# Kernel tuning notes

Hardware: AMD Instinct MI355X
Metric: run time of the kernel (lower is better)

The kernel has to match this reference:

```python
import jax, jax.numpy as jnp
import numpy as np

B_SZ, NX, IN_DIM = 32, 16384, 3
DIM, J, MODE, RANK, FC_DIM, OUT_DIM, N_LAYERS = 64, 16, 128, 4, 128, 1, 3


def setup_inputs() -> dict:
    key = jax.random.key(0)
    ks = jax.random.split(key, 20)
    scale = 1.0 / (MODE * MODE)
    s_out = 1.0 / MODE
    x = jax.random.normal(ks[0], (B_SZ, NX, IN_DIM), jnp.float32)
    bases = jax.random.normal(ks[1], (NX, MODE), jnp.float32) / np.sqrt(NX)
    wbases = jax.random.normal(ks[2], (NX, MODE), jnp.float32) / np.sqrt(NX)
    product = bases.T @ wbases  # (MODE_out, MODE_in)
    D_out = np.sqrt(s_out) * jax.random.uniform(ks[3], (J, MODE), jnp.float32)
    D_in = np.sqrt(s_out) * jax.random.uniform(ks[4], (J, MODE), jnp.float32)
    A = s_out * jax.random.uniform(ks[5], (J, RANK, MODE), jnp.float32)
    Bm = s_out * jax.random.uniform(ks[6], (J, RANK, MODE), jnp.float32)
    W_sp = scale * jax.random.normal(ks[7], (N_LAYERS, DIM, DIM, J), jnp.float32)
    W_conv = jax.random.normal(ks[8], (N_LAYERS, DIM, DIM), jnp.float32) / np.sqrt(DIM)
    b_conv = jnp.zeros((N_LAYERS, DIM), jnp.float32)
    W0 = jax.random.normal(ks[9], (IN_DIM, DIM), jnp.float32) / np.sqrt(IN_DIM)
    b0 = jnp.zeros((DIM,), jnp.float32)
    W1 = jax.random.normal(ks[10], (DIM, FC_DIM), jnp.float32) / np.sqrt(DIM)
    b1 = jnp.zeros((FC_DIM,), jnp.float32)
    W2 = jax.random.normal(ks[11], (FC_DIM, OUT_DIM), jnp.float32) / np.sqrt(FC_DIM)
    b2 = jnp.zeros((OUT_DIM,), jnp.float32)
    return {"x": x, "bases": bases, "wbases": wbases, "product": product,
            "D_out": D_out, "D_in": D_in, "A": A, "Bm": Bm,
            "W_sp": W_sp, "W_conv": W_conv, "b_conv": b_conv,
            "W0": W0, "b0": b0, "W1": W1, "b1": b1, "W2": W2, "b2": b2}


def reference(x, bases, wbases, product, D_out, D_in, A, Bm, W_sp, W_conv, b_conv,
              W0, b0, W1, b1, W2, b2):
    # fc0: (b, nx, in_dim) -> (b, nx, dim), then channel-first (b, dim, nx)
    h = jnp.swapaxes(x @ W0 + b0, 1, 2)
    # H construction: diag outer-products + low-rank A^T B update (mask_mode=0 so full add)
    H = D_out[:, :, None] * D_in[:, None, :] * product[None] \
        + jnp.einsum('jrk,jrl->jkl', A, Bm)  # (J, MODE, MODE)
    for i in range(N_LAYERS):
        xh = jnp.einsum('bcx,xk->bck', h, wbases)          # spectral transform
        xh1 = jnp.einsum('jkl,bil->bijk', H, xh)           # H mixing
        y = jnp.einsum('ioj,bijk->bok', W_sp[i], xh1)      # channel/kernel contraction
        x1 = jnp.einsum('bck,xk->bcx', y, bases)           # inverse transform
        x2 = jnp.einsum('oc,bcx->box', W_conv[i], h) + b_conv[i][None, :, None]
        h = x1 + x2
        if i != N_LAYERS - 1:
            h = jax.nn.gelu(h, approximate=False)
    h = jnp.swapaxes(h, 1, 2)  # (b, nx, dim)
    h = jax.nn.gelu(h @ W1 + b1, approximate=False)
    return h @ W2 + b2
```

## Files before the change

### kernel.cpp

```cpp
#include <hip/hip_runtime.h>
#include <hip/hip_bf16.h>
#include <math.h>

#define B_SZ   32
#define NXX    16384
#define IN_DIM 3
#define DIM    64
#define JM     16
#define MODE   128
#define RANKK  4
#define FC_DIM 128
#define N_LAY  3

typedef __attribute__((ext_vector_type(8))) short bf16x8;
typedef __attribute__((ext_vector_type(4))) float f32x4;
typedef unsigned short u16;

__device__ __forceinline__ float gelu_fast(float v) {
    float p = v * (0.7978845608f + 0.0356774081f * v * v);
    float e = __expf(-2.f * p);
    return v * __builtin_amdgcn_rcpf(1.f + e);
}
__device__ __forceinline__ u16 to_bf16(float v) {
    __hip_bfloat16 b = __float2bfloat16(v);
    return *(u16*)&b;
}

__global__ __launch_bounds__(256) void k_zero(float* __restrict__ p, int n) {
    int i = blockIdx.x * 256 + threadIdx.x;
    if (i < n) p[i] = 0.f;
}

__global__ __launch_bounds__(256) void k_build_H(
        const float* __restrict__ Dout, const float* __restrict__ Din,
        const float* __restrict__ product, const float* __restrict__ A,
        const float* __restrict__ Bm, u16* __restrict__ Hbf) {
    int idx = blockIdx.x * 256 + threadIdx.x;
    int j = idx >> 14;
    int k = (idx >> 7) & 127;
    int l = idx & 127;
    float v = Dout[j * MODE + k] * Din[j * MODE + l] * product[k * MODE + l];
#pragma unroll
    for (int r = 0; r < RANKK; ++r)
        v += A[(j * RANKK + r) * MODE + k] * Bm[(j * RANKK + r) * MODE + l];
    Hbf[idx] = to_bf16(v);
}

__global__ __launch_bounds__(256) void k_setup_wst(
        const float* __restrict__ Wsp, u16* __restrict__ WsT) {
    int idx = blockIdx.x * 256 + threadIdx.x;
    int i = idx & 63, o = (idx >> 6) & 63, j = (idx >> 12) & 15, lay = idx >> 16;
    WsT[idx] = to_bf16(Wsp[(((size_t)lay * 64 + i) * 64 + o) * 16 + j]);
}

__global__ __launch_bounds__(256) void k_setup_bases(
        const float* __restrict__ bases, u16* __restrict__ bh) {
    int idx = blockIdx.x * 256 + threadIdx.x;
    int x = idx >> 7, k = idx & 127;
    size_t off = (size_t)(k >> 3) * 131072 + (size_t)x * 8 + (k & 7);
    bh[off] = to_bf16(bases[idx]);
}

__global__ __launch_bounds__(256) void k_setup_wbT(
        const float* __restrict__ wb, u16* __restrict__ Th) {
    __shared__ float tile[32][33];
    int bx = blockIdx.x, bl = blockIdx.y;
    int t = threadIdx.x;
    int i = t >> 5, jj = t & 31;
#pragma unroll
    for (int r = 0; r < 4; ++r)
        tile[i + r * 8][jj] = wb[(size_t)(bx * 32 + i + r * 8) * MODE + bl * 32 + jj];
    __syncthreads();
#pragma unroll
    for (int r = 0; r < 4; ++r) {
        int l = bl * 32 + i + r * 8;
        int x = bx * 32 + jj;
        Th[(size_t)l * NXX + x] = to_bf16(tile[jj][i + r * 8]);
    }
}

__global__ __launch_bounds__(256) void k_setup_w1t(
        const float* __restrict__ W1, u16* __restrict__ wh) {
    int i = blockIdx.x * 256 + threadIdx.x;
    int f = i >> 6, c = i & 63;
    wh[i] = to_bf16(W1[c * FC_DIM + f]);
}

__global__ __launch_bounds__(256) void k_fc0(
        const float* __restrict__ x, const float* __restrict__ W0,
        const float* __restrict__ b0, u16* __restrict__ hh) {
    __shared__ float w0s[IN_DIM * DIM + DIM];
    int t = threadIdx.x;
    if (t < IN_DIM * DIM) w0s[t] = W0[t];
    if (t < DIM) w0s[IN_DIM * DIM + t] = b0[t];
    __syncthreads();
    int b = blockIdx.y;
    int xi = blockIdx.x * 32 + (t >> 3);
    int c8 = (t & 7) * 8;
    const float* xp = x + ((size_t)b * NXX + xi) * IN_DIM;
    float x0 = xp[0], x1 = xp[1], x2 = xp[2];
    u16 rh[8];
#pragma unroll
    for (int i = 0; i < 8; ++i) {
        int c = c8 + i;
        float v = x0 * w0s[c] + x1 * w0s[DIM + c] + x2 * w0s[2 * DIM + c]
                + w0s[3 * DIM + c];
        rh[i] = to_bf16(v);
    }
    size_t o = ((size_t)(b << 14) + xi) * 64 + c8;
    *(ushort4*)(hh + o)     = make_ushort4(rh[0], rh[1], rh[2], rh[3]);
    *(ushort4*)(hh + o + 4) = make_ushort4(rh[4], rh[5], rh[6], rh[7]);
}

#define SPAD 72
__global__ __launch_bounds__(256) void k_spectral_mfma(
        const u16* __restrict__ Hh,
        const u16* __restrict__ Wh,
        float* __restrict__ xh) {
    __shared__ u16 Ash[64 * SPAD];
    int t = threadIdx.x;
    int wave = t >> 6, lane = t & 63, quad = lane >> 4, l16 = lane & 15;
    int b = blockIdx.x;
    int x0 = blockIdx.y * 512;
    int cq = (t & 15) * 4;
    int xq = (t >> 4) * 4;
    int colw = (xq + ((t & 7) << 3)) & 63;
    const u16* srch = Hh + ((size_t)(b << 14) + x0 + xq) * 64 + cq;
    int l0 = wave * 32;
    const u16* w0h = Wh + (size_t)(l0 + l16) * NXX + x0;
    const u16* w1h = Wh + (size_t)(l0 + 16 + l16) * NXX + x0;
    f32x4 acc[4][2] = {};
    for (int kt = 0; kt < 512; kt += 64) {
        __syncthreads();
        {
            const u16* s = srch + (size_t)kt * 64;
            ushort4 r0 = *(const ushort4*)(s);
            ushort4 r1 = *(const ushort4*)(s + 64);
            ushort4 r2 = *(const ushort4*)(s + 128);
            ushort4 r3 = *(const ushort4*)(s + 192);
            *(ushort4*)&Ash[(cq + 0) * SPAD + colw] = make_ushort4(r0.x, r1.x, r2.x, r3.x);
            *(ushort4*)&Ash[(cq + 1) * SPAD + colw] = make_ushort4(r0.y, r1.y, r2.y, r3.y);
            *(ushort4*)&Ash[(cq + 2) * SPAD + colw] = make_ushort4(r0.z, r1.z, r2.z, r3.z);
            *(ushort4*)&Ash[(cq + 3) * SPAD + colw] = make_ushort4(r0.w, r1.w, r2.w, r3.w);
        }
        __syncthreads();
#pragma unroll
        for (int k0 = 0; k0 < 64; k0 += 32) {
            bf16x8 afh[4];
#pragma unroll
            for (int ct = 0; ct < 4; ++ct) {
                int rr = ct * 16 + l16;
                int ro = rr * SPAD + (((k0 + quad * 8) + (((rr >> 2) & 7) << 3)) & 63);
                afh[ct] = *(const bf16x8*)&Ash[ro];
            }
            int go = kt + k0 + quad * 8;
            bf16x8 b0h = *(const bf16x8*)(w0h + go);
            bf16x8 b1h = *(const bf16x8*)(w1h + go);
#pragma unroll
            for (int ct = 0; ct < 4; ++ct) {
                acc[ct][0] = __builtin_amdgcn_mfma_f32_16x16x32_bf16(afh[ct], b0h, acc[ct][0], 0, 0, 0);
                acc[ct][1] = __builtin_amdgcn_mfma_f32_16x16x32_bf16(afh[ct], b1h, acc[ct][1], 0, 0, 0);
            }
        }
    }
    float* xb = xh + (size_t)(b << 6) * 128;
#pragma unroll
    for (int ct = 0; ct < 4; ++ct)
#pragma unroll
        for (int lt = 0; lt < 2; ++lt)
#pragma unroll
            for (int r = 0; r < 4; ++r)
                atomicAdd(xb + (size_t)(ct * 16 + quad * 4 + r) * 128 + l0 + lt * 16 + l16,
                          acc[ct][lt][r]);
}

#define XPAD 136
#define TPAD 72
__global__ __launch_bounds__(256) void k_hmix_mfma(
        const float* __restrict__ xh, const u16* __restrict__ Hbf,
        const u16* __restrict__ WsT, float* __restrict__ y, int lay) {
    __shared__ u16 xsb[64 * XPAD];
    __shared__ u16 Ts[128 * TPAD];
    int t = threadIdx.x;
    int wave = t >> 6, lane = t & 63, quad = lane >> 4, l16 = lane & 15;
    int b = blockIdx.x, j = blockIdx.y;
    const float* xb = xh + (size_t)b * DIM * MODE;
    for (int idx = t; idx < DIM * MODE; idx += 256)
        xsb[(idx >> 7) * XPAD + (idx & 127)] = to_bf16(xb[idx]);
    __syncthreads();
    int k_base = wave * 32;
    {
        f32x4 acc[2][4] = {};
        const u16* Hj = Hbf + (size_t)j * MODE * MODE;
#pragma unroll
        for (int l0 = 0; l0 < 128; l0 += 32) {
            bf16x8 af[2], bf[4];
#pragma unroll
            for (int mt = 0; mt < 2; ++mt)
                af[mt] = *(const bf16x8*)(Hj + (size_t)(k_base + mt * 16 + l16) * 128 + l0 + quad * 8);
#pragma unroll
            for (int nt = 0; nt < 4; ++nt)
                bf[nt] = *(const bf16x8*)&xsb[(nt * 16 + l16) * XPAD + l0 + quad * 8];
#pragma unroll
            for (int mt = 0; mt < 2; ++mt)
#pragma unroll
                for (int nt = 0; nt < 4; ++nt)
                    acc[mt][nt] = __builtin_amdgcn_mfma_f32_16x16x32_bf16(af[mt], bf[nt], acc[mt][nt], 0, 0, 0);
        }
#pragma unroll
        for (int mt = 0; mt < 2; ++mt)
#pragma unroll
            for (int nt = 0; nt < 4; ++nt)
#pragma unroll
                for (int r = 0; r < 4; ++r)
                    Ts[(k_base + mt * 16 + quad * 4 + r) * TPAD + nt * 16 + l16] =
                        to_bf16(acc[mt][nt][r]);
    }
    __syncthreads();
    {
        f32x4 acc[4][2] = {};
        const u16* Wj = WsT + ((size_t)lay * JM + j) * DIM * DIM;
#pragma unroll
        for (int i0 = 0; i0 < 64; i0 += 32) {
            bf16x8 af[4], bf[2];
#pragma unroll
            for (int mt = 0; mt < 4; ++mt)
                af[mt] = *(const bf16x8*)(Wj + (size_t)(mt * 16 + l16) * 64 + i0 + quad * 8);
#pragma unroll
            for (int nt = 0; nt < 2; ++nt)
                bf[nt] = *(const bf16x8*)&Ts[(k_base + nt * 16 + l16) * TPAD + i0 + quad * 8];
#pragma unroll
            for (int mt = 0; mt < 4; ++mt)
#pragma unroll
                for (int nt = 0; nt < 2; ++nt)
                    acc[mt][nt] = __builtin_amdgcn_mfma_f32_16x16x32_bf16(af[mt], bf[nt], acc[mt][nt], 0, 0, 0);
        }
        float* yb = y + (size_t)b * DIM * MODE;
#pragma unroll
        for (int mt = 0; mt < 4; ++mt)
#pragma unroll
            for (int nt = 0; nt < 2; ++nt)
#pragma unroll
                for (int r = 0; r < 4; ++r)
                    atomicAdd(yb + (size_t)(mt * 16 + quad * 4 + r) * 128 + k_base + nt * 16 + l16,
                              acc[mt][nt][r]);
    }
}

__global__ __launch_bounds__(256) void k_build_A(
        const float* __restrict__ y, const float* __restrict__ Wconv,
        u16* __restrict__ Ah, int lay) {
    int b = blockIdx.x;
    for (int idx = threadIdx.x; idx < 12288; idx += 256) {
        int i = idx & 7, l16 = (idx >> 3) & 15, quad = (idx >> 7) & 3,
            ot = (idx >> 9) & 3, ks = idx >> 11;
        int o = ot * 16 + l16;
        int k = ks * 32 + quad * 8 + i;
        float v = (k < 128) ? y[((size_t)b * DIM + o) * MODE + k]
                            : Wconv[(size_t)lay * DIM * DIM + o * DIM + (k - 128)];
        Ah[(size_t)b * 12288 + idx] = to_bf16(v);
    }
}

#define CPAD 72
template <bool DO_MLP>
__global__ __launch_bounds__(256, 4) void k_inv_conv_mfma(
        const u16* __restrict__ Afh,
        const u16* __restrict__ Bfh,
        u16* __restrict__ Hh,
        const float* __restrict__ bconv, int lay,
        const u16* __restrict__ W1h,
        const float* __restrict__ b1, const float* __restrict__ W2,
        const float* __restrict__ b2, float* __restrict__ out) {
    __shared__ u16 hsh[128 * CPAD];
    int t = threadIdx.x;
    int wave = t >> 6, lane = t & 63, quad = lane >> 4, l16 = lane & 15;
    int b = blockIdx.x;
    int x0 = blockIdx.y * 128;
#pragma unroll
    for (int it = 0; it < 4; ++it) {
        int idx = it * 256 + t;
        int row = idx >> 3, c8 = (idx & 7) * 8;
        size_t src = ((size_t)(b << 14) + x0 + row) * 64 + c8;
        *(bf16x8*)&hsh[row * CPAD + c8] = *(const bf16x8*)(Hh + src);
    }
    __syncthreads();

    int xw = wave * 32;
    const u16* afb_h = Afh + (size_t)b * 12288;
    f32x4 acc[4][2] = {};
#pragma unroll
    for (int ks = 0; ks < 6; ++ks) {
        bf16x8 afh[4], bfh[2];
#pragma unroll
        for (int ot = 0; ot < 4; ++ot) {
            size_t ao = (size_t)(((ks * 4 + ot) * 4 + quad) * 16 + l16) * 8;
            afh[ot] = *(const bf16x8*)(afb_h + ao);
        }
#pragma unroll
        for (int x2 = 0; x2 < 2; ++x2) {
            int xl = xw + x2 * 16 + l16;
            if (ks < 4) {
                size_t bo = (size_t)((ks * 4 + quad) * 16384 + x0 + xl) * 8;
                bfh[x2] = *(const bf16x8*)(Bfh + bo);
            } else {
                int ko = (ks - 4) * 32 + quad * 8;
                bfh[x2] = *(const bf16x8*)&hsh[xl * CPAD + ko];
            }
        }
#pragma unroll
        for (int ot = 0; ot < 4; ++ot)
#pragma unroll
            for (int x2 = 0; x2 < 2; ++x2)
                acc[ot][x2] = __builtin_amdgcn_mfma_f32_16x16x32_bf16(afh[ot], bfh[x2], acc[ot][x2], 0, 0, 0);
    }
    __syncthreads();

#pragma unroll
    for (int ot = 0; ot < 4; ++ot) {
        float4 bc = *(const float4*)(bconv + lay * DIM + ot * 16 + quad * 4);
#pragma unroll
        for (int x2 = 0; x2 < 2; ++x2) {
            int xl = xw + x2 * 16 + l16;
            float vr[4] = {acc[ot][x2][0] + bc.x, acc[ot][x2][1] + bc.y,
                           acc[ot][x2][2] + bc.z, acc[ot][x2][3] + bc.w};
            if (!DO_MLP) {
#pragma unroll
                for (int r = 0; r < 4; ++r) vr[r] = gelu_fast(vr[r]);
            }
            ushort4 uh;
            uh.x = to_bf16(vr[0]); uh.y = to_bf16(vr[1]);
            uh.z = to_bf16(vr[2]); uh.w = to_bf16(vr[3]);
            *(ushort4*)&hsh[xl * CPAD + ot * 16 + quad * 4] = uh;
        }
    }
    __syncthreads();

    if (!DO_MLP) {
#pragma unroll
        for (int it = 0; it < 4; ++it) {
            int idx = it * 256 + t;
            int row = idx >> 3, c8 = (idx & 7) * 8;
            size_t dst = ((size_t)(b << 14) + x0 + row) * 64 + c8;
            *(bf16x8*)(Hh + dst) = *(const bf16x8*)&hsh[row * CPAD + c8];
        }
        return;
    }

#pragma unroll
    for (int x2 = 0; x2 < 2; ++x2) {
        bf16x8 ah[2];
#pragma unroll
        for (int ks = 0; ks < 2; ++ks) {
            int ro = (xw + x2 * 16 + l16) * CPAD + ks * 32 + quad * 8;
            ah[ks] = *(const bf16x8*)&hsh[ro];
        }
        float vo[4] = {0.f, 0.f, 0.f, 0.f};
#pragma unroll
        for (int ft = 0; ft < 8; ++ft) {
            f32x4 a2 = {};
#pragma unroll
            for (int ks = 0; ks < 2; ++ks) {
                size_t o = (size_t)(ft * 16 + l16) * 64 + ks * 32 + quad * 8;
                bf16x8 bh = *(const bf16x8*)(W1h + o);
                a2 = __builtin_amdgcn_mfma_f32_16x16x32_bf16(ah[ks], bh, a2, 0, 0, 0);
            }
            float bb = b1[ft * 16 + l16];
            float w2 = W2[ft * 16 + l16];
#pragma unroll
            for (int r = 0; r < 4; ++r)
                vo[r] += gelu_fast(a2[r] + bb) * w2;
        }
#pragma unroll
        for (int r = 0; r < 4; ++r) {
            float v = vo[r];
            v += __shfl_xor(v, 1);
            v += __shfl_xor(v, 2);
            v += __shfl_xor(v, 4);
            v += __shfl_xor(v, 8);
            vo[r] = v;
        }
        if (l16 == 0) {
            float bb2 = b2[0];
            float4 o4 = make_float4(vo[0] + bb2, vo[1] + bb2, vo[2] + bb2, vo[3] + bb2);
            *(float4*)(out + (size_t)b * NXX + x0 + xw + x2 * 16 + quad * 4) = o4;
        }
    }
}

extern "C" void kernel_launch(void* const* d_in, const int* in_sizes, int n_in,
                              void* d_out, int out_size, void* d_ws, size_t ws_size,
                              hipStream_t stream) {
    const float* x      = (const float*)d_in[0];
    const float* bases  = (const float*)d_in[1];
    const float* wbases = (const float*)d_in[2];
    const float* product= (const float*)d_in[3];
    const float* Dout   = (const float*)d_in[4];
    const float* Din    = (const float*)d_in[5];
    const float* A      = (const float*)d_in[6];
    const float* Bm     = (const float*)d_in[7];
    const float* Wsp    = (const float*)d_in[8];
    const float* Wconv  = (const float*)d_in[9];
    const float* bconv  = (const float*)d_in[10];
    const float* W0     = (const float*)d_in[11];
    const float* b0     = (const float*)d_in[12];
    const float* W1     = (const float*)d_in[13];
    const float* b1     = (const float*)d_in[14];
    const float* W2     = (const float*)d_in[15];
    const float* b2     = (const float*)d_in[16];
    float* out = (float*)d_out;

    const size_t need = 79314944;
    if (ws_size < need) {
        k_zero<<<dim3((out_size + 255) / 256), dim3(256), 0, stream>>>(out, out_size);
        return;
    }

    char* W = (char*)d_ws;
    size_t off = 0;
    auto alloc = [&](size_t bytes) { void* p = W + off; off += bytes; return p; };
    u16*   Hbf      = (u16*)alloc(524288);
    u16*   WsT      = (u16*)alloc(393216);
    u16*   bases_hi = (u16*)alloc(4194304);
    u16*   wbT_hi   = (u16*)alloc(4194304);
    u16*   Abuf_hi  = (u16*)alloc(786432);
    float* ybuf     = (float*)alloc(1048576);
    float* xh       = (float*)alloc(1048576);
    u16*   h_hi     = (u16*)alloc(67108864);
    u16*   w1t_hi   = (u16*)alloc(16384);

    k_build_H<<<dim3(1024), dim3(256), 0, stream>>>(Dout, Din, product, A, Bm, Hbf);
    k_setup_wst<<<dim3(768), dim3(256), 0, stream>>>(Wsp, WsT);
    k_setup_bases<<<dim3(8192), dim3(256), 0, stream>>>(bases, bases_hi);
    k_setup_wbT<<<dim3(512, 4), dim3(256), 0, stream>>>(wbases, wbT_hi);
    k_setup_w1t<<<dim3(32), dim3(256), 0, stream>>>(W1, w1t_hi);
    k_fc0<<<dim3(512, B_SZ), dim3(256), 0, stream>>>(x, W0, b0, h_hi);

    for (int lay = 0; lay < N_LAY; ++lay) {
        int last = (lay == N_LAY - 1);
        k_zero<<<dim3(2048), dim3(256), 0, stream>>>(ybuf, 524288);
        k_spectral_mfma<<<dim3(B_SZ, 32), dim3(256), 0, stream>>>(
            h_hi, wbT_hi, xh);
        k_hmix_mfma<<<dim3(B_SZ, JM), dim3(256), 0, stream>>>(
            xh, Hbf, WsT, ybuf, lay);
        k_build_A<<<dim3(B_SZ), dim3(256), 0, stream>>>(ybuf, Wconv, Abuf_hi, lay);
        dim3 g(B_SZ, 128), blk(256);
        if (last)
            k_inv_conv_mfma<true><<<g, blk, 0, stream>>>(
                Abuf_hi, bases_hi, h_hi, bconv, lay,
                w1t_hi, b1, W2, b2, out);
        else
            k_inv_conv_mfma<false><<<g, blk, 0, stream>>>(
                Abuf_hi, bases_hi, h_hi, bconv, lay,
                w1t_hi, b1, W2, b2, out);
    }
}
```

Before: 499.7 us.

## Stage per-batch A matrix in LDS and loop each block over four x-tiles

The inverse-transform/conv kernel now copies the per-batch A operand (12288 bf16) into shared memory once and reuses it across four 128-point x tiles per block, cutting the grid from 128 to 32 blocks along x. It also drops the LDS staging of the H tile: the conv operand is read straight from global memory and the GELU output is written straight to global with 8-byte stores. This is meant to cut repeated global A loads and block-level barriers. In exchange it launches fewer blocks, which may lower occupancy and latency hiding, and the global stores are less coalesced.

```diff
diff --git a/kernel.cpp b/kernel.cpp
--- a/kernel.cpp
+++ b/kernel.cpp
@@ -272,118 +272,115 @@
         const u16* __restrict__ W1h,
         const float* __restrict__ b1, const float* __restrict__ W2,
         const float* __restrict__ b2, float* __restrict__ out) {
-    __shared__ u16 hsh[128 * CPAD];
+    __shared__ u16 Ash[12288];
+    __shared__ u16 osh[DO_MLP ? 128 * CPAD : 8];
     int t = threadIdx.x;
     int wave = t >> 6, lane = t & 63, quad = lane >> 4, l16 = lane & 15;
     int b = blockIdx.x;
-    int x0 = blockIdx.y * 128;
-#pragma unroll
-    for (int it = 0; it < 4; ++it) {
-        int idx = it * 256 + t;
-        int row = idx >> 3, c8 = (idx & 7) * 8;
-        size_t src = ((size_t)(b << 14) + x0 + row) * 64 + c8;
-        *(bf16x8*)&hsh[row * CPAD + c8] = *(const bf16x8*)(Hh + src);
+    int xs = blockIdx.y * 512;
+
+    const u16* afb = Afh + (size_t)b * 12288;
+#pragma unroll
+    for (int i = 0; i < 6; ++i) {
+        int idx = i * 256 + t;
+        *(bf16x8*)&Ash[idx * 8] = *(const bf16x8*)(afb + (size_t)idx * 8);
     }
     __syncthreads();
 
     int xw = wave * 32;
-    const u16* afb_h = Afh + (size_t)b * 12288;
-    f32x4 acc[4][2] = {};
-#pragma unroll
-    for (int ks = 0; ks < 6; ++ks) {
-        bf16x8 afh[4], bfh[2];
+#pragma unroll 2
+    for (int xt = 0; xt < 4; ++xt) {
+        int x0 = xs + xt * 128;
+        f32x4 acc[4][2] = {};
+#pragma unroll
+        for (int ks = 0; ks < 6; ++ks) {
+            bf16x8 afh[4], bfh[2];
+#pragma unroll
+            for (int x2 = 0; x2 < 2; ++x2) {
+                int xl = xw + x2 * 16 + l16;
+                if (ks < 4) {
+                    size_t bo = (size_t)((ks * 4 + quad) * 16384 + x0 + xl) * 8;
+                    bfh[x2] = *(const bf16x8*)(Bfh + bo);
+                } else {
+                    int ko = (ks - 4) * 32 + quad * 8;
+                    bfh[x2] = *(const bf16x8*)(Hh + ((size_t)(b << 14) + x0 + xl) * 64 + ko);
+                }
+            }
+#pragma unroll
+            for (int ot = 0; ot < 4; ++ot)
+                afh[ot] = *(const bf16x8*)&Ash[(((ks * 4 + ot) * 4 + quad) * 16 + l16) * 8];
+#pragma unroll
+            for (int ot = 0; ot < 4; ++ot)
+#pragma unroll
+                for (int x2 = 0; x2 < 2; ++x2)
+                    acc[ot][x2] = __builtin_amdgcn_mfma_f32_16x16x32_bf16(
+                        afh[ot], bfh[x2], acc[ot][x2], 0, 0, 0);
+        }
+
 #pragma unroll
         for (int ot = 0; ot < 4; ++ot) {
-            size_t ao = (size_t)(((ks * 4 + ot) * 4 + quad) * 16 + l16) * 8;
-            afh[ot] = *(const bf16x8*)(afb_h + ao);
-        }
-#pragma unroll
-        for (int x2 = 0; x2 < 2; ++x2) {
-            int xl = xw + x2 * 16 + l16;
-            if (ks < 4) {
-                size_t bo = (size_t)((ks * 4 + quad) * 16384 + x0 + xl) * 8;
-                bfh[x2] = *(const bf16x8*)(Bfh + bo);
-            } else {
-                int ko = (ks - 4) * 32 + quad * 8;
-                bfh[x2] = *(const bf16x8*)&hsh[xl * CPAD + ko];
+            float4 bc = *(const float4*)(bconv + lay * DIM + ot * 16 + quad * 4);
+#pragma unroll
+            for (int x2 = 0; x2 < 2; ++x2) {
+                int xl = xw + x2 * 16 + l16;
+                float vr[4] = {acc[ot][x2][0] + bc.x, acc[ot][x2][1] + bc.y,
+                               acc[ot][x2][2] + bc.z, acc[ot][x2][3] + bc.w};
+                ushort4 uh;
+                if (!DO_MLP) {
+                    uh.x = to_bf16(gelu_fast(vr[0]));
+                    uh.y = to_bf16(gelu_fast(vr[1]));
+                    uh.z = to_bf16(gelu_fast(vr[2]));
+                    uh.w = to_bf16(gelu_fast(vr[3]));
+                    *(ushort4*)(Hh + ((size_t)(b << 14) + x0 + xl) * 64 + ot * 16 + quad * 4) = uh;
+                } else {
+                    uh.x = to_bf16(vr[0]); uh.y = to_bf16(vr[1]);
+                    uh.z = to_bf16(vr[2]); uh.w = to_bf16(vr[3]);
+                    *(ushort4*)&osh[xl * CPAD + ot * 16 + quad * 4] = uh;
+                }
             }
         }
-#pragma unroll
-        for (int ot = 0; ot < 4; ++ot)
-#pragma unroll
-            for (int x2 = 0; x2 < 2; ++x2)
-                acc[ot][x2] = __builtin_amdgcn_mfma_f32_16x16x32_bf16(afh[ot], bfh[x2], acc[ot][x2], 0, 0, 0);
-    }
-    __syncthreads();
-
-#pragma unroll
-    for (int ot = 0; ot < 4; ++ot) {
-        float4 bc = *(const float4*)(bconv + lay * DIM + ot * 16 + quad * 4);
-#pragma unroll
-        for (int x2 = 0; x2 < 2; ++x2) {
-            int xl = xw + x2 * 16 + l16;
-            float vr[4] = {acc[ot][x2][0] + bc.x, acc[ot][x2][1] + bc.y,
-                           acc[ot][x2][2] + bc.z, acc[ot][x2][3] + bc.w};
-            if (!DO_MLP) {
-#pragma unroll
-                for (int r = 0; r < 4; ++r) vr[r] = gelu_fast(vr[r]);
+
+        if (DO_MLP) {
+#pragma unroll
+            for (int x2 = 0; x2 < 2; ++x2) {
+                bf16x8 ah[2];
+#pragma unroll
+                for (int ks = 0; ks < 2; ++ks) {
+                    int ro = (xw + x2 * 16 + l16) * CPAD + ks * 32 + quad * 8;
+                    ah[ks] = *(const bf16x8*)&osh[ro];
+                }
+                float vo[4] = {0.f, 0.f, 0.f, 0.f};
+#pragma unroll
+                for (int ft = 0; ft < 8; ++ft) {
+                    f32x4 a2 = {};
+#pragma unroll
+                    for (int ks = 0; ks < 2; ++ks) {
+                        size_t o = (size_t)(ft * 16 + l16) * 64 + ks * 32 + quad * 8;
+                        bf16x8 bh = *(const bf16x8*)(W1h + o);
+                        a2 = __builtin_amdgcn_mfma_f32_16x16x32_bf16(ah[ks], bh, a2, 0, 0, 0);
+                    }
+                    float bb = b1[ft * 16 + l16];
+                    float w2 = W2[ft * 16 + l16];
+#pragma unroll
+                    for (int r = 0; r < 4; ++r)
+                        vo[r] += gelu_fast(a2[r] + bb) * w2;
+                }
+#pragma unroll
+                for (int r = 0; r < 4; ++r) {
+                    float v = vo[r];
+                    v += __shfl_xor(v, 1);
+                    v += __shfl_xor(v, 2);
+                    v += __shfl_xor(v, 4);
+                    v += __shfl_xor(v, 8);
+                    vo[r] = v;
+                }
+                if (l16 == 0) {
+                    float bb2 = b2[0];
+                    float4 o4 = make_float4(vo[0] + bb2, vo[1] + bb2,
+                                            vo[2] + bb2, vo[3] + bb2);
+                    *(float4*)(out + (size_t)b * NXX + x0 + xw + x2 * 16 + quad * 4) = o4;
+                }
             }
-            ushort4 uh;
-            uh.x = to_bf16(vr[0]); uh.y = to_bf16(vr[1]);
-            uh.z = to_bf16(vr[2]); uh.w = to_bf16(vr[3]);
-            *(ushort4*)&hsh[xl * CPAD + ot * 16 + quad * 4] = uh;
-        }
-    }
-    __syncthreads();
-
-    if (!DO_MLP) {
-#pragma unroll
-        for (int it = 0; it < 4; ++it) {
-            int idx = it * 256 + t;
-            int row = idx >> 3, c8 = (idx & 7) * 8;
-            size_t dst = ((size_t)(b << 14) + x0 + row) * 64 + c8;
-            *(bf16x8*)(Hh + dst) = *(const bf16x8*)&hsh[row * CPAD + c8];
-        }
-        return;
-    }
-
-#pragma unroll
-    for (int x2 = 0; x2 < 2; ++x2) {
-        bf16x8 ah[2];
-#pragma unroll
-        for (int ks = 0; ks < 2; ++ks) {
-            int ro = (xw + x2 * 16 + l16) * CPAD + ks * 32 + quad * 8;
-            ah[ks] = *(const bf16x8*)&hsh[ro];
-        }
-        float vo[4] = {0.f, 0.f, 0.f, 0.f};
-#pragma unroll
-        for (int ft = 0; ft < 8; ++ft) {
-            f32x4 a2 = {};
-#pragma unroll
-            for (int ks = 0; ks < 2; ++ks) {
-                size_t o = (size_t)(ft * 16 + l16) * 64 + ks * 32 + quad * 8;
-                bf16x8 bh = *(const bf16x8*)(W1h + o);
-                a2 = __builtin_amdgcn_mfma_f32_16x16x32_bf16(ah[ks], bh, a2, 0, 0, 0);
-            }
-            float bb = b1[ft * 16 + l16];
-            float w2 = W2[ft * 16 + l16];
-#pragma unroll
-            for (int r = 0; r < 4; ++r)
-                vo[r] += gelu_fast(a2[r] + bb) * w2;
-        }
-#pragma unroll
-        for (int r = 0; r < 4; ++r) {
-            float v = vo[r];
-            v += __shfl_xor(v, 1);
-            v += __shfl_xor(v, 2);
-            v += __shfl_xor(v, 4);
-            v += __shfl_xor(v, 8);
-            vo[r] = v;
-        }
-        if (l16 == 0) {
-            float bb2 = b2[0];
-            float4 o4 = make_float4(vo[0] + bb2, vo[1] + bb2, vo[2] + bb2, vo[3] + bb2);
-            *(float4*)(out + (size_t)b * NXX + x0 + xw + x2 * 16 + quad * 4) = o4;
         }
     }
 }
@@ -444,7 +441,7 @@
         k_hmix_mfma<<<dim3(B_SZ, JM), dim3(256), 0, stream>>>(
             xh, Hbf, WsT, ybuf, lay);
         k_build_A<<<dim3(B_SZ), dim3(256), 0, stream>>>(ybuf, Wconv, Abuf_hi, lay);
-        dim3 g(B_SZ, 128), blk(256);
+        dim3 g(B_SZ, 32), blk(256);
         if (last)
             k_inv_conv_mfma<true><<<g, blk, 0, stream>>>(
                 Abuf_hi, bases_hi, h_hi, bconv, lay,
```

Result: slower. 626.6 us (+25.4%).

## Stage A tile in LDS, swizzle h tile, remap blocks for L2 locality

Applied to the files above, without the earlier changes.

The inverse-transform/conv kernel now copies the per-batch A operand into shared memory once per block instead of having every wave read it from global memory. The padded h tile is replaced by an XOR-swizzled 64-wide layout, so bank conflicts are avoided without padding. The grid becomes 1-D with an index remap so that blocks landing on the same XCD share x-tiles of the bases matrix across batches. The basis-fragment loads are hoisted ahead of the MFMA loop and two barriers are removed, since each wave only touches its own rows. Shared-memory use per block rises to about 40 KB, which could limit occupancy.

```diff
diff --git a/kernel.cpp b/kernel.cpp
--- a/kernel.cpp
+++ b/kernel.cpp
@@ -262,7 +262,6 @@
     }
 }
 
-#define CPAD 72
 template <bool DO_MLP>
 __global__ __launch_bounds__(256, 4) void k_inv_conv_mfma(
         const u16* __restrict__ Afh,
@@ -272,49 +271,66 @@
         const u16* __restrict__ W1h,
         const float* __restrict__ b1, const float* __restrict__ W2,
         const float* __restrict__ b2, float* __restrict__ out) {
-    __shared__ u16 hsh[128 * CPAD];
+    __shared__ u16 Ash[12288];
+    __shared__ u16 hsh[128 * 64];
     int t = threadIdx.x;
     int wave = t >> 6, lane = t & 63, quad = lane >> 4, l16 = lane & 15;
-    int b = blockIdx.x;
-    int x0 = blockIdx.y * 128;
+    int bid = blockIdx.x;
+    int swz = (bid & 7) * 512 + (bid >> 3);
+    int b = swz & 31;
+    int x0 = (swz >> 5) * 128;
+
+    const u16* afb = Afh + (size_t)b * 12288;
+#pragma unroll
+    for (int i = 0; i < 6; ++i) {
+        int idx = i * 256 + t;
+        *(bf16x8*)&Ash[idx * 8] = *(const bf16x8*)(afb + (size_t)idx * 8);
+    }
 #pragma unroll
     for (int it = 0; it < 4; ++it) {
         int idx = it * 256 + t;
         int row = idx >> 3, c8 = (idx & 7) * 8;
         size_t src = ((size_t)(b << 14) + x0 + row) * 64 + c8;
-        *(bf16x8*)&hsh[row * CPAD + c8] = *(const bf16x8*)(Hh + src);
+        *(bf16x8*)&hsh[row * 64 + (c8 ^ ((row & 7) << 3))] =
+            *(const bf16x8*)(Hh + src);
     }
     __syncthreads();
 
     int xw = wave * 32;
-    const u16* afb_h = Afh + (size_t)b * 12288;
+    bf16x8 bglob[4][2];
+#pragma unroll
+    for (int ks = 0; ks < 4; ++ks)
+#pragma unroll
+        for (int x2 = 0; x2 < 2; ++x2) {
+            int xl = xw + x2 * 16 + l16;
+            size_t bo = (size_t)((ks * 4 + quad) * 16384 + x0 + xl) * 8;
+            bglob[ks][x2] = *(const bf16x8*)(Bfh + bo);
+        }
+
     f32x4 acc[4][2] = {};
 #pragma unroll
     for (int ks = 0; ks < 6; ++ks) {
         bf16x8 afh[4], bfh[2];
 #pragma unroll
-        for (int ot = 0; ot < 4; ++ot) {
-            size_t ao = (size_t)(((ks * 4 + ot) * 4 + quad) * 16 + l16) * 8;
-            afh[ot] = *(const bf16x8*)(afb_h + ao);
-        }
-#pragma unroll
         for (int x2 = 0; x2 < 2; ++x2) {
-            int xl = xw + x2 * 16 + l16;
             if (ks < 4) {
-                size_t bo = (size_t)((ks * 4 + quad) * 16384 + x0 + xl) * 8;
-                bfh[x2] = *(const bf16x8*)(Bfh + bo);
+                bfh[x2] = bglob[ks][x2];
             } else {
+                int xl = xw + x2 * 16 + l16;
                 int ko = (ks - 4) * 32 + quad * 8;
-                bfh[x2] = *(const bf16x8*)&hsh[xl * CPAD + ko];
+                bfh[x2] = *(const bf16x8*)&hsh[xl * 64 + (ko ^ ((xl & 7) << 3))];
             }
         }
 #pragma unroll
         for (int ot = 0; ot < 4; ++ot)
+            afh[ot] = *(const bf16x8*)&Ash[(((ks * 4 + ot) * 4 + quad) * 16 + l16) * 8];
+#pragma unroll
+        for (int ot = 0; ot < 4; ++ot)
 #pragma unroll
             for (int x2 = 0; x2 < 2; ++x2)
-                acc[ot][x2] = __builtin_amdgcn_mfma_f32_16x16x32_bf16(afh[ot], bfh[x2], acc[ot][x2], 0, 0, 0);
-    }
-    __syncthreads();
+                acc[ot][x2] = __builtin_amdgcn_mfma_f32_16x16x32_bf16(
+                    afh[ot], bfh[x2], acc[ot][x2], 0, 0, 0);
+    }
 
 #pragma unroll
     for (int ot = 0; ot < 4; ++ot) {
@@ -331,29 +347,32 @@
             ushort4 uh;
             uh.x = to_bf16(vr[0]); uh.y = to_bf16(vr[1]);
             uh.z = to_bf16(vr[2]); uh.w = to_bf16(vr[3]);
-            *(ushort4*)&hsh[xl * CPAD + ot * 16 + quad * 4] = uh;
-        }
-    }
-    __syncthreads();
+            int col = ot * 16 + quad * 4;
+            *(ushort4*)&hsh[xl * 64 + (col ^ ((xl & 7) << 3))] = uh;
+        }
+    }
 
     if (!DO_MLP) {
+        __syncthreads();
 #pragma unroll
         for (int it = 0; it < 4; ++it) {
             int idx = it * 256 + t;
             int row = idx >> 3, c8 = (idx & 7) * 8;
             size_t dst = ((size_t)(b << 14) + x0 + row) * 64 + c8;
-            *(bf16x8*)(Hh + dst) = *(const bf16x8*)&hsh[row * CPAD + c8];
+            *(bf16x8*)(Hh + dst) =
+                *(const bf16x8*)&hsh[row * 64 + (c8 ^ ((row & 7) << 3))];
         }
         return;
     }
 
 #pragma unroll
     for (int x2 = 0; x2 < 2; ++x2) {
+        int xl = xw + x2 * 16 + l16;
         bf16x8 ah[2];
 #pragma unroll
         for (int ks = 0; ks < 2; ++ks) {
-            int ro = (xw + x2 * 16 + l16) * CPAD + ks * 32 + quad * 8;
-            ah[ks] = *(const bf16x8*)&hsh[ro];
+            int ko = ks * 32 + quad * 8;
+            ah[ks] = *(const bf16x8*)&hsh[xl * 64 + (ko ^ ((xl & 7) << 3))];
         }
         float vo[4] = {0.f, 0.f, 0.f, 0.f};
 #pragma unroll
@@ -382,7 +401,8 @@
         }
         if (l16 == 0) {
             float bb2 = b2[0];
-            float4 o4 = make_float4(vo[0] + bb2, vo[1] + bb2, vo[2] + bb2, vo[3] + bb2);
+            float4 o4 = make_float4(vo[0] + bb2, vo[1] + bb2,
+                                    vo[2] + bb2, vo[3] + bb2);
             *(float4*)(out + (size_t)b * NXX + x0 + xw + x2 * 16 + quad * 4) = o4;
         }
     }
@@ -444,7 +464,7 @@
         k_hmix_mfma<<<dim3(B_SZ, JM), dim3(256), 0, stream>>>(
             xh, Hbf, WsT, ybuf, lay);
         k_build_A<<<dim3(B_SZ), dim3(256), 0, stream>>>(ybuf, Wconv, Abuf_hi, lay);
-        dim3 g(B_SZ, 128), blk(256);
+        dim3 g(4096), blk(256);
         if (last)
             k_inv_conv_mfma<true><<<g, blk, 0, stream>>>(
                 Abuf_hi, bases_hi, h_hi, bconv, lay,
```

After: 473.9 us. 5.2% less time.
